# Optimization experiments

Measured on AMD Instinct MI355X. Metric: run time of the kernel, lower is better.

The kernel has to match this reference:

```python
import jax, jax.numpy as jnp
import numpy as np

B, H, W, C = 4, 256, 256, 64
KH = KW = 3
UNITS = 1          # forced: conv in-channels must equal kernel in-channels (see notes)
G = 1              # num_deformable_group
HP, WP = H + 2, W + 2  # 'same' padding for 3x3 stride-1: pad 1 each side


def _conv_indices(h, w):
    """Replicates tf.image.extract_image_patches('SAME') on an index grid:
    border patches read zero-padded coordinates. Returns int [h, w, 9]."""
    yg, xg = jnp.meshgrid(jnp.arange(h), jnp.arange(w), indexing='ij')
    yp = jnp.pad(yg, 1)
    xp = jnp.pad(xg, 1)
    ys = jnp.stack([yp[ky:ky + h, kx:kx + w] for ky in range(KH) for kx in range(KW)], -1)
    xs = jnp.stack([xp[ky:ky + h, kx:kx + w] for ky in range(KH) for kx in range(KW)], -1)
    return ys, xs


def setup_inputs() -> dict:
    key = jax.random.key(0)
    k1, k2, k3, k4 = jax.random.split(key, 4)
    input_fp = jax.random.normal(k1, (B, H, W, C), jnp.float32)
    gt_mask = jax.random.randint(k2, (1, H, W, 1), 0, 2).astype(jnp.float32)
    offset = jax.random.normal(k3, (B, H, W, UNITS * KH * KW * 2), jnp.float32)
    fan_in = KH * KW * C
    kernel = jax.random.normal(k4, (KH, KW, C, UNITS), jnp.float32) / np.float32(np.sqrt(fan_in))
    bias = jnp.zeros((UNITS,), jnp.float32)
    return {"input_fp": input_fp, "gt_mask": gt_mask, "offset": offset,
            "kernel": kernel, "bias": bias}


def reference(input_fp, gt_mask, offset, kernel, bias):
    pad = ((0, 0), (1, 1), (1, 1), (0, 0))
    fp = jnp.pad(input_fp, pad)                 # [B, HP, WP, C]
    mk = jnp.pad(gt_mask, pad)[0, :, :, 0]      # [HP, WP]; original tiles this over batch/channels

    off = offset.reshape(B, H, W, UNITS * KH * KW, 2)
    y_off, x_off = off[..., 0], off[..., 1]     # [B, H, W, 9]

    yi, xi = _conv_indices(H, W)                # [H, W, 9] int
    yf = yi[None].astype(jnp.float32)           # [1, H, W, 9], broadcasts over batch
    xf = xi[None].astype(jnp.float32)

    # mask at base sample points and at offset sample points
    p_mask = mk[yi, xi][None]                                        # [1, H, W, 9]
    yo = jnp.clip(jnp.floor(yf + y_off).astype(jnp.int32), 0, HP - 1)
    xo = jnp.clip(jnp.floor(xf + x_off).astype(jnp.int32), 0, WP - 1)
    p_mask_off = mk[yo, xo]                                          # [B, H, W, 9]
    diff = (p_mask != p_mask_off).astype(jnp.float32)

    y = jnp.clip(yf + y_off * diff, 0.0, H - 1.0)
    x = jnp.clip(xf + x_off * diff, 0.0, W - 1.0)
    y0 = jnp.floor(y).astype(jnp.int32)
    x0 = jnp.floor(x).astype(jnp.int32)

    b = jnp.arange(B)[:, None, None, None]
    pixels = fp[b, y0, x0]                      # [B, H, W, 9, C] nearest-floor sampling
    # [B,H,W,kh,kw,G,C] -> [B,H,kh,W,kw,G,C] -> [B, H*kh, W*kw, G*C]
    pixels = pixels.reshape(B, H, W, KH, KW, G, C)
    pixels = pixels.transpose(0, 1, 3, 2, 4, 5, 6)
    pixels = pixels.reshape(B, H * KH, W * KW, G * C)   # feat_in_group = units//G = 1, tile is a no-op

    out = jax.lax.conv_general_dilated(
        pixels, kernel, window_strides=(KH, KW), padding='SAME',
        dimension_numbers=('NHWC', 'HWIO', 'NHWC'))      # [B, H, W, UNITS]
    return out + bias
```

## Files before the change

### kernel.cpp

```cpp
#include <hip/hip_runtime.h>

#define HW 256
#define CH 64

__global__ __launch_bounds__(256, 6) void DeformableConvLayer_kernel(
    const float* __restrict__ inp,
    const float* __restrict__ gt,
    const float* __restrict__ off,
    const float* __restrict__ ker,
    const float* __restrict__ bias,
    float* __restrict__ out)
{
    __shared__ float wlds[576];
    const int tid = threadIdx.x;
    if (tid < 144) ((float4*)wlds)[tid] = ((const float4*)ker)[tid];

    const int lane = tid & 63;
    const int wave = tid >> 6;
    const int q16  = lane & 48;
    const int t    = lane & 15;

    const int bid = blockIdx.x;
    const int vb  = (bid & 7) * 2048 + (bid >> 3);

    const int p = vb * 16 + wave * 4 + (q16 >> 4);
    const int b = p >> 16;
    const int i = (p >> 8) & 255;
    const int j = p & 255;
    const float* inb = inp + (long)b * (HW * HW * CH);

    int pack = 0;
    if (t < 9) {
        const int tap = t;
        const int ky = tap / 3, kx = tap - ky * 3;
        int iy = i + ky - 1, ix = j + kx - 1;
        bool interior = (iy >= 0) & (iy < HW) & (ix >= 0) & (ix < HW);
        int yi = interior ? iy : 0;
        int xi = interior ? ix : 0;

        float p_mask = (yi >= 1 && xi >= 1) ? gt[(yi - 1) * HW + (xi - 1)] : 0.f;

        float2 o2 = *(const float2*)(off + (long)p * 18 + 2 * tap);
        float yf = (float)yi, xf = (float)xi;

        float yof = fminf(fmaxf(floorf(yf + o2.x), 0.f), 257.f);
        float xof = fminf(fmaxf(floorf(xf + o2.y), 0.f), 257.f);
        int yo = (int)yof, xo = (int)xof;
        float p_mask_off = (yo >= 1 && yo <= HW && xo >= 1 && xo <= HW)
                           ? gt[(yo - 1) * HW + (xo - 1)] : 0.f;
        float diff = (p_mask != p_mask_off) ? 1.f : 0.f;

        float y = fminf(fmaxf(yf + o2.x * diff, 0.f), 255.f);
        float x = fminf(fmaxf(xf + o2.y * diff, 0.f), 255.f);
        int y0 = (int)y;
        int x0 = (int)x;

        bool valid = (y0 >= 1) & (x0 >= 1);
        int eoff = ((y0 - 1) * HW + (x0 - 1)) * CH;
        pack = valid ? eoff : -1;
    }

    int pk[9];
    #pragma unroll
    for (int k = 0; k < 9; ++k) pk[k] = __shfl(pack, q16 + k);

    float4 v[9];
    #pragma unroll
    for (int k = 0; k < 9; ++k) {
        int eo = pk[k] >= 0 ? pk[k] : 0;
        v[k] = *(const float4*)(inb + eo + t * 4);
    }

    __syncthreads();

    float acc = 0.f;
    #pragma unroll
    for (int k = 0; k < 9; ++k) {
        float s = pk[k] >= 0 ? 1.f : 0.f;
        float4 w = ((const float4*)wlds)[k * 16 + t];
        float d = v[k].x * w.x + v[k].y * w.y + v[k].z * w.z + v[k].w * w.w;
        acc = fmaf(s, d, acc);
    }

    acc += __shfl_xor(acc, 8);
    acc += __shfl_xor(acc, 4);
    acc += __shfl_xor(acc, 2);
    acc += __shfl_xor(acc, 1);
    if (t == 0) out[p] = acc + bias[0];
}

extern "C" void kernel_launch(void* const* d_in, const int* in_sizes, int n_in,
                              void* d_out, int out_size, void* d_ws, size_t ws_size,
                              hipStream_t stream) {
    const float* inp  = (const float*)d_in[0];
    const float* gt   = (const float*)d_in[1];
    const float* off  = (const float*)d_in[2];
    const float* ker  = (const float*)d_in[3];
    const float* bias = (const float*)d_in[4];
    float* out = (float*)d_out;

    DeformableConvLayer_kernel<<<16384, 256, 0, stream>>>(inp, gt, off, ker, bias, out);
}
```

Baseline: 134.3 us.

## Process two output pixels per 16-lane group with software-pipelined gathers

Each 16-lane group now computes two output pixels, four columns apart. The second pixel's gather loads are issued while the first pixel's dot products are accumulated, which halves the grid and amortizes the per-block weight load into LDS. Occupancy bound rises from 6 to 8, and the 0/1 scaling multiply is replaced by a validity bitmask select. Register pressure from holding two sets of offsets and loads at the higher occupancy bound risks spills.

```diff
diff --git a/kernel.cpp b/kernel.cpp
--- a/kernel.cpp
+++ b/kernel.cpp
@@ -3,7 +3,7 @@
 #define HW 256
 #define CH 64
 
-__global__ __launch_bounds__(256, 6) void DeformableConvLayer_kernel(
+__global__ __launch_bounds__(256, 8) void DeformableConvLayer_kernel(
     const float* __restrict__ inp,
     const float* __restrict__ gt,
     const float* __restrict__ off,
@@ -21,72 +21,115 @@
     const int t    = lane & 15;
 
     const int bid = blockIdx.x;
-    const int vb  = (bid & 7) * 2048 + (bid >> 3);
+    const int vb  = (bid & 7) * 1024 + (bid >> 3);
 
-    const int p = vb * 16 + wave * 4 + (q16 >> 4);
-    const int b = p >> 16;
-    const int i = (p >> 8) & 255;
-    const int j = p & 255;
+    const int p0 = vb * 32 + wave * 8 + (q16 >> 4);
+    const int p1 = p0 + 4;
+    const int b  = p0 >> 16;
+    const int i  = (p0 >> 8) & 255;
+    const int j0 = p0 & 255;
+    const int j1 = j0 + 4;
     const float* inb = inp + (long)b * (HW * HW * CH);
 
-    int pack = 0;
+    int pack0 = -1, pack1 = -1;
     if (t < 9) {
         const int tap = t;
         const int ky = tap / 3, kx = tap - ky * 3;
-        int iy = i + ky - 1, ix = j + kx - 1;
-        bool interior = (iy >= 0) & (iy < HW) & (ix >= 0) & (ix < HW);
-        int yi = interior ? iy : 0;
-        int xi = interior ? ix : 0;
+        const int iy = i + ky - 1;
 
-        float p_mask = (yi >= 1 && xi >= 1) ? gt[(yi - 1) * HW + (xi - 1)] : 0.f;
+        float2 oa = *(const float2*)(off + (long)p0 * 18 + 2 * tap);
+        float2 ob = *(const float2*)(off + (long)p1 * 18 + 2 * tap);
 
-        float2 o2 = *(const float2*)(off + (long)p * 18 + 2 * tap);
-        float yf = (float)yi, xf = (float)xi;
-
-        float yof = fminf(fmaxf(floorf(yf + o2.x), 0.f), 257.f);
-        float xof = fminf(fmaxf(floorf(xf + o2.y), 0.f), 257.f);
-        int yo = (int)yof, xo = (int)xof;
-        float p_mask_off = (yo >= 1 && yo <= HW && xo >= 1 && xo <= HW)
-                           ? gt[(yo - 1) * HW + (xo - 1)] : 0.f;
-        float diff = (p_mask != p_mask_off) ? 1.f : 0.f;
-
-        float y = fminf(fmaxf(yf + o2.x * diff, 0.f), 255.f);
-        float x = fminf(fmaxf(xf + o2.y * diff, 0.f), 255.f);
-        int y0 = (int)y;
-        int x0 = (int)x;
-
-        bool valid = (y0 >= 1) & (x0 >= 1);
-        int eoff = ((y0 - 1) * HW + (x0 - 1)) * CH;
-        pack = valid ? eoff : -1;
+        {
+            int ix = j0 + kx - 1;
+            bool interior = (iy >= 0) & (iy < HW) & (ix >= 0) & (ix < HW);
+            int yi = interior ? iy : 0;
+            int xi = interior ? ix : 0;
+            float p_mask = (yi >= 1 && xi >= 1) ? gt[(yi - 1) * HW + (xi - 1)] : 0.f;
+            float yf = (float)yi, xf = (float)xi;
+            float yof = fminf(fmaxf(floorf(yf + oa.x), 0.f), 257.f);
+            float xof = fminf(fmaxf(floorf(xf + oa.y), 0.f), 257.f);
+            int yo = (int)yof, xo = (int)xof;
+            float p_mask_off = (yo >= 1 && yo <= HW && xo >= 1 && xo <= HW)
+                               ? gt[(yo - 1) * HW + (xo - 1)] : 0.f;
+            float diff = (p_mask != p_mask_off) ? 1.f : 0.f;
+            float y = fminf(fmaxf(yf + oa.x * diff, 0.f), 255.f);
+            float x = fminf(fmaxf(xf + oa.y * diff, 0.f), 255.f);
+            int y0 = (int)y, x0 = (int)x;
+            bool valid = (y0 >= 1) & (x0 >= 1);
+            pack0 = valid ? ((y0 - 1) * HW + (x0 - 1)) * CH : -1;
+        }
+        {
+            int ix = j1 + kx - 1;
+            bool interior = (iy >= 0) & (iy < HW) & (ix >= 0) & (ix < HW);
+            int yi = interior ? iy : 0;
+            int xi = interior ? ix : 0;
+            float p_mask = (yi >= 1 && xi >= 1) ? gt[(yi - 1) * HW + (xi - 1)] : 0.f;
+            float yf = (float)yi, xf = (float)xi;
+            float yof = fminf(fmaxf(floorf(yf + ob.x), 0.f), 257.f);
+            float xof = fminf(fmaxf(floorf(xf + ob.y), 0.f), 257.f);
+            int yo = (int)yof, xo = (int)xof;
+            float p_mask_off = (yo >= 1 && yo <= HW && xo >= 1 && xo <= HW)
+                               ? gt[(yo - 1) * HW + (xo - 1)] : 0.f;
+            float diff = (p_mask != p_mask_off) ? 1.f : 0.f;
+            float y = fminf(fmaxf(yf + ob.x * diff, 0.f), 255.f);
+            float x = fminf(fmaxf(xf + ob.y * diff, 0.f), 255.f);
+            int y0 = (int)y, x0 = (int)x;
+            bool valid = (y0 >= 1) & (x0 >= 1);
+            pack1 = valid ? ((y0 - 1) * HW + (x0 - 1)) * CH : -1;
+        }
     }
 
-    int pk[9];
+    int pk0[9];
     #pragma unroll
-    for (int k = 0; k < 9; ++k) pk[k] = __shfl(pack, q16 + k);
+    for (int k = 0; k < 9; ++k) pk0[k] = __shfl(pack0, q16 + k);
 
     float4 v[9];
     #pragma unroll
     for (int k = 0; k < 9; ++k) {
-        int eo = pk[k] >= 0 ? pk[k] : 0;
+        int eo = pk0[k] >= 0 ? pk0[k] : 0;
+        v[k] = *(const float4*)(inb + eo + t * 4);
+    }
+    int m0 = 0;
+    #pragma unroll
+    for (int k = 0; k < 9; ++k) m0 |= (int)(pk0[k] >= 0) << k;
+
+    int pk1[9];
+    #pragma unroll
+    for (int k = 0; k < 9; ++k) pk1[k] = __shfl(pack1, q16 + k);
+
+    __syncthreads();
+
+    float acc0 = 0.f;
+    int m1 = 0;
+    #pragma unroll
+    for (int k = 0; k < 9; ++k) {
+        float4 w = ((const float4*)wlds)[k * 16 + t];
+        float d = v[k].x * w.x + v[k].y * w.y + v[k].z * w.z + v[k].w * w.w;
+        acc0 += ((m0 >> k) & 1) ? d : 0.f;
+        m1 |= (int)(pk1[k] >= 0) << k;
+        int eo = pk1[k] >= 0 ? pk1[k] : 0;
         v[k] = *(const float4*)(inb + eo + t * 4);
     }
 
-    __syncthreads();
+    acc0 += __shfl_xor(acc0, 8);
+    acc0 += __shfl_xor(acc0, 4);
+    acc0 += __shfl_xor(acc0, 2);
+    acc0 += __shfl_xor(acc0, 1);
+    if (t == 0) out[p0] = acc0 + bias[0];
 
-    float acc = 0.f;
+    float acc1 = 0.f;
     #pragma unroll
     for (int k = 0; k < 9; ++k) {
-        float s = pk[k] >= 0 ? 1.f : 0.f;
         float4 w = ((const float4*)wlds)[k * 16 + t];
         float d = v[k].x * w.x + v[k].y * w.y + v[k].z * w.z + v[k].w * w.w;
-        acc = fmaf(s, d, acc);
+        acc1 += ((m1 >> k) & 1) ? d : 0.f;
     }
-
-    acc += __shfl_xor(acc, 8);
-    acc += __shfl_xor(acc, 4);
-    acc += __shfl_xor(acc, 2);
-    acc += __shfl_xor(acc, 1);
-    if (t == 0) out[p] = acc + bias[0];
+    acc1 += __shfl_xor(acc1, 8);
+    acc1 += __shfl_xor(acc1, 4);
+    acc1 += __shfl_xor(acc1, 2);
+    acc1 += __shfl_xor(acc1, 1);
+    if (t == 0) out[p1] = acc1 + bias[0];
 }
 
 extern "C" void kernel_launch(void* const* d_in, const int* in_sizes, int n_in,
@@ -99,5 +142,5 @@
     const float* bias = (const float*)d_in[4];
     float* out = (float*)d_out;
 
-    DeformableConvLayer_kernel<<<16384, 256, 0, stream>>>(inp, gt, off, ker, bias, out);
+    DeformableConvLayer_kernel<<<8192, 256, 0, stream>>>(inp, gt, off, ker, bias, out);
 }
```

After: 135.1 us. About the same (+0.5%).

## Split coordinate computation into separate kernel writing packed sample indices

Applied to the files above, without the earlier changes.

Splits the fused kernel into two passes. The first computes per-tap floor sample coordinates with one thread per (pixel, tap) and stores them as packed 16-bit values in the workspace. The second loads these packed indices and does the gather plus dot product with all lanes busy. This removes the 7-of-16 idle lanes and the shuffles in the coordinate phase, at the cost of an extra launch and a workspace round-trip. The original fused path is kept as a fallback when no workspace is supplied.

```diff
diff --git a/kernel.cpp b/kernel.cpp
--- a/kernel.cpp
+++ b/kernel.cpp
@@ -2,14 +2,115 @@
 
 #define HW 256
 #define CH 64
-
-__global__ __launch_bounds__(256, 6) void DeformableConvLayer_kernel(
-    const float* __restrict__ inp,
+#define NPIX (4 * HW * HW)
+#define WS_BYTES ((size_t)NPIX * 24)
+
+__global__ __launch_bounds__(256, 8) void DeformA_kernel(
     const float* __restrict__ gt,
     const float* __restrict__ off,
+    unsigned short* __restrict__ ws)
+{
+    const unsigned g = blockIdx.x * 256u + threadIdx.x;
+    const unsigned p = g / 9u;
+    const int tap = (int)(g - p * 9u);
+    const int i = (int)((p >> 8) & 255u);
+    const int j = (int)(p & 255u);
+    const int ky = tap / 3, kx = tap - ky * 3;
+
+    const float2 o2 = *(const float2*)(off + (size_t)g * 2);
+
+    const int iy = i + ky - 1, ix = j + kx - 1;
+    const bool interior = (iy >= 0) & (iy < HW) & (ix >= 0) & (ix < HW);
+    const int yi = interior ? iy : 0;
+    const int xi = interior ? ix : 0;
+    const float p_mask = (yi >= 1 && xi >= 1) ? gt[(yi - 1) * HW + (xi - 1)] : 0.f;
+
+    const float yf = (float)yi, xf = (float)xi;
+    const float yof = fminf(fmaxf(floorf(yf + o2.x), 0.f), 257.f);
+    const float xof = fminf(fmaxf(floorf(xf + o2.y), 0.f), 257.f);
+    const int yo = (int)yof, xo = (int)xof;
+    const float p_mask_off = (yo >= 1 && yo <= HW && xo >= 1 && xo <= HW)
+                             ? gt[(yo - 1) * HW + (xo - 1)] : 0.f;
+    const float diff = (p_mask != p_mask_off) ? 1.f : 0.f;
+    const float y = fminf(fmaxf(yf + o2.x * diff, 0.f), 255.f);
+    const float x = fminf(fmaxf(xf + o2.y * diff, 0.f), 255.f);
+    const int y0 = (int)y, x0 = (int)x;
+
+    ws[p * 12u + (unsigned)tap] = (unsigned short)((y0 << 8) | x0);
+}
+
+__global__ __launch_bounds__(256, 4) void DeformB_kernel(
+    const float* __restrict__ inp,
+    const unsigned short* __restrict__ ws,
     const float* __restrict__ ker,
     const float* __restrict__ bias,
     float* __restrict__ out)
+{
+    __shared__ float wlds[576];
+    const int tid = threadIdx.x;
+    if (tid < 144) ((float4*)wlds)[tid] = ((const float4*)ker)[tid];
+
+    const int lane = tid & 63;
+    const int wave = tid >> 6;
+    const int t = lane & 15;
+
+    const int bid = blockIdx.x;
+    const int vb = (bid & 7) * 2048 + (bid >> 3);
+    const int p = vb * 16 + wave * 4 + (lane >> 4);
+
+    const int bb = __builtin_amdgcn_readfirstlane(p >> 16);
+    const float* inb = inp + (size_t)bb * (HW * HW * CH);
+
+    const uint2* e = (const uint2*)(ws + (size_t)p * 12u);
+    const uint2 eA = e[0];
+    const uint2 eB = e[1];
+    const unsigned eC = *(const unsigned*)(e + 2);
+
+    unsigned enc[9];
+    enc[0] = eA.x & 0xffffu; enc[1] = eA.x >> 16;
+    enc[2] = eA.y & 0xffffu; enc[3] = eA.y >> 16;
+    enc[4] = eB.x & 0xffffu; enc[5] = eB.x >> 16;
+    enc[6] = eB.y & 0xffffu; enc[7] = eB.y >> 16;
+    enc[8] = eC & 0xffffu;
+
+    int m = 0;
+    int eo[9];
+    #pragma unroll
+    for (int k = 0; k < 9; ++k) {
+        const int yy = (int)(enc[k] >> 8);
+        const int xx = (int)(enc[k] & 255u);
+        const bool valid = (yy >= 1) & (xx >= 1);
+        m |= (int)valid << k;
+        eo[k] = valid ? ((yy - 1) * HW + (xx - 1)) * CH : 0;
+    }
+
+    const int co = t * 4;
+    float4 v[9];
+    #pragma unroll
+    for (int k = 0; k < 9; ++k)
+        v[k] = *(const float4*)(inb + eo[k] + co);
+
+    __syncthreads();
+
+    float acc = 0.f;
+    #pragma unroll
+    for (int k = 0; k < 9; ++k) {
+        const float4 w = ((const float4*)wlds)[k * 16 + t];
+        const float d = v[k].x * w.x + v[k].y * w.y + v[k].z * w.z + v[k].w * w.w;
+        acc += ((m >> k) & 1) ? d : 0.f;
+    }
+
+    acc += __shfl_xor(acc, 8);
+    acc += __shfl_xor(acc, 4);
+    acc += __shfl_xor(acc, 2);
+    acc += __shfl_xor(acc, 1);
+    if (t == 0) out[p] = acc + bias[0];
+}
+
+__global__ __launch_bounds__(256, 6) void DeformFallback_kernel(
+    const float* __restrict__ inp, const float* __restrict__ gt,
+    const float* __restrict__ off, const float* __restrict__ ker,
+    const float* __restrict__ bias, float* __restrict__ out)
 {
     __shared__ float wlds[576];
     const int tid = threadIdx.x;
@@ -37,24 +138,19 @@
         bool interior = (iy >= 0) & (iy < HW) & (ix >= 0) & (ix < HW);
         int yi = interior ? iy : 0;
         int xi = interior ? ix : 0;
-
         float p_mask = (yi >= 1 && xi >= 1) ? gt[(yi - 1) * HW + (xi - 1)] : 0.f;
-
         float2 o2 = *(const float2*)(off + (long)p * 18 + 2 * tap);
         float yf = (float)yi, xf = (float)xi;
-
         float yof = fminf(fmaxf(floorf(yf + o2.x), 0.f), 257.f);
         float xof = fminf(fmaxf(floorf(xf + o2.y), 0.f), 257.f);
         int yo = (int)yof, xo = (int)xof;
         float p_mask_off = (yo >= 1 && yo <= HW && xo >= 1 && xo <= HW)
                            ? gt[(yo - 1) * HW + (xo - 1)] : 0.f;
         float diff = (p_mask != p_mask_off) ? 1.f : 0.f;
-
         float y = fminf(fmaxf(yf + o2.x * diff, 0.f), 255.f);
         float x = fminf(fmaxf(xf + o2.y * diff, 0.f), 255.f);
         int y0 = (int)y;
         int x0 = (int)x;
-
         bool valid = (y0 >= 1) & (x0 >= 1);
         int eoff = ((y0 - 1) * HW + (x0 - 1)) * CH;
         pack = valid ? eoff : -1;
@@ -67,8 +163,8 @@
     float4 v[9];
     #pragma unroll
     for (int k = 0; k < 9; ++k) {
-        int eo = pk[k] >= 0 ? pk[k] : 0;
-        v[k] = *(const float4*)(inb + eo + t * 4);
+        int eo2 = pk[k] >= 0 ? pk[k] : 0;
+        v[k] = *(const float4*)(inb + eo2 + t * 4);
     }
 
     __syncthreads();
@@ -99,5 +195,11 @@
     const float* bias = (const float*)d_in[4];
     float* out = (float*)d_out;
 
-    DeformableConvLayer_kernel<<<16384, 256, 0, stream>>>(inp, gt, off, ker, bias, out);
-}
+    if (d_ws != nullptr && ws_size >= WS_BYTES) {
+        DeformA_kernel<<<9216, 256, 0, stream>>>(gt, off, (unsigned short*)d_ws);
+        DeformB_kernel<<<16384, 256, 0, stream>>>(
+            inp, (const unsigned short*)d_ws, ker, bias, out);
+    } else {
+        DeformFallback_kernel<<<16384, 256, 0, stream>>>(inp, gt, off, ker, bias, out);
+    }
+}
```

Result: no change. 136.6 us (+1.7%).

## Precompute per-pixel tap dot products, then gather scalars in a second kernel

Applied to the files above, without the earlier changes.

Because UNITS is 1, the gathered 64-channel vectors can be reduced against each tap's weights ahead of time. A first kernel computes, for every input pixel, its dot product with all nine tap weight vectors and stores them in a 12-float workspace table. A second kernel then gathers one scalar per tap instead of a 256-byte channel vector. This removes the large random channel gathers but adds a 12.6 MB workspace write and read plus a second launch, and falls back to the original kernel when no workspace is provided.

```diff
diff --git a/kernel.cpp b/kernel.cpp
--- a/kernel.cpp
+++ b/kernel.cpp
@@ -2,14 +2,116 @@
 
 #define HW 256
 #define CH 64
-
-__global__ __launch_bounds__(256, 6) void DeformableConvLayer_kernel(
+#define NPIX (4 * HW * HW)
+#define DM_BYTES ((size_t)NPIX * 48)
+
+__global__ __launch_bounds__(256, 8) void DeformD_kernel(
     const float* __restrict__ inp,
+    const float* __restrict__ ker,
+    float* __restrict__ dm)
+{
+    __shared__ float wlds[576];
+    const int tid = threadIdx.x;
+    if (tid < 144) ((float4*)wlds)[tid] = ((const float4*)ker)[tid];
+    const float4* wq = (const float4*)wlds;
+
+    const int lane = tid & 63;
+    const int wave = tid >> 6;
+    const int t = lane & 15;
+    const int g = lane >> 4;
+
+    const int p0 = blockIdx.x * 32 + (wave * 4 + g) * 2;
+
+    const float4 v0 = *(const float4*)(inp + (size_t)p0 * 64 + t * 4);
+    const float4 v1 = *(const float4*)(inp + (size_t)(p0 + 1) * 64 + t * 4);
+
+    __syncthreads();
+
+    float da[9], db[9];
+    #pragma unroll
+    for (int k = 0; k < 9; ++k) {
+        const float4 w = wq[k * 16 + t];
+        da[k] = v0.x * w.x + v0.y * w.y + v0.z * w.z + v0.w * w.w;
+        db[k] = v1.x * w.x + v1.y * w.y + v1.z * w.z + v1.w * w.w;
+    }
+    #pragma unroll
+    for (int k = 0; k < 9; ++k) {
+        da[k] += __shfl_xor(da[k], 8);
+        da[k] += __shfl_xor(da[k], 4);
+        da[k] += __shfl_xor(da[k], 2);
+        da[k] += __shfl_xor(da[k], 1);
+        db[k] += __shfl_xor(db[k], 8);
+        db[k] += __shfl_xor(db[k], 4);
+        db[k] += __shfl_xor(db[k], 2);
+        db[k] += __shfl_xor(db[k], 1);
+    }
+    float sa = da[8], sb = db[8];
+    #pragma unroll
+    for (int k = 7; k >= 0; --k) {
+        sa = (t == k) ? da[k] : sa;
+        sb = (t == k) ? db[k] : sb;
+    }
+    if (t < 9) {
+        dm[(size_t)p0 * 12 + t] = sa;
+        dm[(size_t)(p0 + 1) * 12 + t] = sb;
+    }
+}
+
+__global__ __launch_bounds__(256, 4) void DeformC_kernel(
     const float* __restrict__ gt,
     const float* __restrict__ off,
-    const float* __restrict__ ker,
+    const float* __restrict__ dm,
     const float* __restrict__ bias,
     float* __restrict__ out)
+{
+    const int tid = threadIdx.x;
+    const int bid = blockIdx.x;
+    const int vb = (bid & 7) * 128 + (bid >> 3);
+    const int p = vb * 256 + tid;
+    const int b = p >> 16;
+    const int i = (p >> 8) & 255;
+    const int j = p & 255;
+
+    const float* offp = off + (size_t)p * 18;
+    float2 o[9];
+    #pragma unroll
+    for (int tap = 0; tap < 9; ++tap)
+        o[tap] = *(const float2*)(offp + 2 * tap);
+
+    const float* dmb = dm + (size_t)(b << 16) * 12;
+
+    float sum = 0.f;
+    #pragma unroll
+    for (int tap = 0; tap < 9; ++tap) {
+        const int ky = tap / 3, kx = tap - ky * 3;
+        const int iy = i + ky - 1, ix = j + kx - 1;
+        const bool interior = (iy >= 0) & (iy < HW) & (ix >= 0) & (ix < HW);
+        const int yi = interior ? iy : 0;
+        const int xi = interior ? ix : 0;
+        const float p_mask = (yi >= 1 && xi >= 1) ? gt[(yi - 1) * HW + (xi - 1)] : 0.f;
+
+        const float yf = (float)yi, xf = (float)xi;
+        const float yof = fminf(fmaxf(floorf(yf + o[tap].x), 0.f), 257.f);
+        const float xof = fminf(fmaxf(floorf(xf + o[tap].y), 0.f), 257.f);
+        const int yo = (int)yof, xo = (int)xof;
+        const float p_mask_off = (yo >= 1 && yo <= HW && xo >= 1 && xo <= HW)
+                                 ? gt[(yo - 1) * HW + (xo - 1)] : 0.f;
+        const float diff = (p_mask != p_mask_off) ? 1.f : 0.f;
+        const float y = fminf(fmaxf(yf + o[tap].x * diff, 0.f), 255.f);
+        const float x = fminf(fmaxf(xf + o[tap].y * diff, 0.f), 255.f);
+        const int y0 = (int)y, x0 = (int)x;
+        const bool valid = (y0 >= 1) & (x0 >= 1);
+        const int idx = valid ? ((y0 - 1) * HW + (x0 - 1)) : 0;
+        const float dval = dmb[(size_t)idx * 12 + tap];
+        sum += valid ? dval : 0.f;
+    }
+    out[p] = sum + bias[0];
+}
+
+__global__ __launch_bounds__(256, 6) void DeformFallback_kernel(
+    const float* __restrict__ inp, const float* __restrict__ gt,
+    const float* __restrict__ off, const float* __restrict__ ker,
+    const float* __restrict__ bias, float* __restrict__ out)
 {
     __shared__ float wlds[576];
     const int tid = threadIdx.x;
@@ -37,24 +139,19 @@
         bool interior = (iy >= 0) & (iy < HW) & (ix >= 0) & (ix < HW);
         int yi = interior ? iy : 0;
         int xi = interior ? ix : 0;
-
         float p_mask = (yi >= 1 && xi >= 1) ? gt[(yi - 1) * HW + (xi - 1)] : 0.f;
-
         float2 o2 = *(const float2*)(off + (long)p * 18 + 2 * tap);
         float yf = (float)yi, xf = (float)xi;
-
         float yof = fminf(fmaxf(floorf(yf + o2.x), 0.f), 257.f);
         float xof = fminf(fmaxf(floorf(xf + o2.y), 0.f), 257.f);
         int yo = (int)yof, xo = (int)xof;
         float p_mask_off = (yo >= 1 && yo <= HW && xo >= 1 && xo <= HW)
                            ? gt[(yo - 1) * HW + (xo - 1)] : 0.f;
         float diff = (p_mask != p_mask_off) ? 1.f : 0.f;
-
         float y = fminf(fmaxf(yf + o2.x * diff, 0.f), 255.f);
         float x = fminf(fmaxf(xf + o2.y * diff, 0.f), 255.f);
         int y0 = (int)y;
         int x0 = (int)x;
-
         bool valid = (y0 >= 1) & (x0 >= 1);
         int eoff = ((y0 - 1) * HW + (x0 - 1)) * CH;
         pack = valid ? eoff : -1;
@@ -67,8 +164,8 @@
     float4 v[9];
     #pragma unroll
     for (int k = 0; k < 9; ++k) {
-        int eo = pk[k] >= 0 ? pk[k] : 0;
-        v[k] = *(const float4*)(inb + eo + t * 4);
+        int eo2 = pk[k] >= 0 ? pk[k] : 0;
+        v[k] = *(const float4*)(inb + eo2 + t * 4);
     }
 
     __syncthreads();
@@ -99,5 +196,10 @@
     const float* bias = (const float*)d_in[4];
     float* out = (float*)d_out;
 
-    DeformableConvLayer_kernel<<<16384, 256, 0, stream>>>(inp, gt, off, ker, bias, out);
-}
+    if (d_ws != nullptr && ws_size >= DM_BYTES) {
+        DeformD_kernel<<<8192, 256, 0, stream>>>(inp, ker, (float*)d_ws);
+        DeformC_kernel<<<1024, 256, 0, stream>>>(gt, off, (const float*)d_ws, bias, out);
+    } else {
+        DeformFallback_kernel<<<16384, 256, 0, stream>>>(inp, gt, off, ker, bias, out);
+    }
+}
```

Result: no change. 135.3 us (+0.7%).
